# Optimization experiments

Measured on AMD Instinct MI355X. Metric: run time of the kernel, lower is better.

Reference implementation:

```python
import jax, jax.numpy as jnp
import numpy as np

B, T, SD, NE = 4, 2048, 64, 4096   # batch, block_size, sqrt_d, n_embd (= SD*SD)
H, HS = 8, 8                        # n_head, head_size (H*HS == SD)
FH = 4 * SD                         # FFN hidden
EPS = 1e-5


def setup_inputs() -> dict:
    key = jax.random.key(0)
    ks = jax.random.split(key, 17)
    s = 0.05  # linear-layer init scale
    return {
        "x": jax.random.normal(ks[0], (B, T, NE), jnp.float32),
        # Feebler / Booster weights: torch.randn in original
        "feebler_w": jax.random.normal(ks[1], (SD, SD, T), jnp.float32),
        "booster_w": jax.random.normal(ks[2], (SD, SD, T), jnp.float32),
        # per-head q/k/v projections (no bias): applied as y @ W -> (B,T,HS)
        "wq": jax.random.normal(ks[3], (H, SD, HS), jnp.float32) * s,
        "wk": jax.random.normal(ks[4], (H, SD, HS), jnp.float32) * s,
        "wv": jax.random.normal(ks[5], (H, SD, HS), jnp.float32) * s,
        "proj_w": jax.random.normal(ks[6], (SD, SD), jnp.float32) * s,
        "proj_b": jnp.zeros((SD,), jnp.float32),
        "ln1_g": jnp.ones((SD,), jnp.float32),
        "ln1_b": jnp.zeros((SD,), jnp.float32),
        "ln2_g": jnp.ones((SD,), jnp.float32),
        "ln2_b": jnp.zeros((SD,), jnp.float32),
        "w1": jax.random.normal(ks[7], (SD, FH), jnp.float32) * s,
        "b1": jnp.zeros((FH,), jnp.float32),
        "w2": jax.random.normal(ks[8], (FH, SD), jnp.float32) * s,
        "b2": jnp.zeros((SD,), jnp.float32),
    }


def _layer_norm(x, g, b):
    m = jnp.mean(x, axis=-1, keepdims=True)
    v = jnp.mean((x - m) ** 2, axis=-1, keepdims=True)
    return (x - m) * jax.lax.rsqrt(v + EPS) * g + b


def reference(x, feebler_w, booster_w, wq, wk, wv, proj_w, proj_b,
              ln1_g, ln1_b, ln2_g, ln2_b, w1, b1, w2, b2):
    # ---- Feebler: (B,T,NE) flat-reshaped to (B,SD,SD,T), mul weights, sum dim 2
    xr = x.reshape(B, SD, SD, T)                     # flat reinterpretation (torch .view)
    h = jnp.einsum('bijt,ijt->bit', xr, feebler_w)   # (B, SD, T)
    h = h.reshape(B, T, SD)                          # flat reinterpretation, NOT transpose

    # ---- QuickHead multi-head 'attention' (sum-pooled elementwise)
    y = _layer_norm(h, ln1_g, ln1_b)                 # (B, T, SD)
    q = jnp.einsum('bts,hsd->bhtd', y, wq)           # (B, H, T, HS)
    k = jnp.einsum('bts,hsd->bhtd', y, wk)
    v = jnp.einsum('bts,hsd->bhtd', y, wv)
    ck = jnp.sum(k, axis=2, keepdims=True)           # (B, H, 1, HS)
    cv = jnp.sum(v, axis=2, keepdims=True)
    aw = jax.nn.softmax(q * ck, axis=2)              # softmax over T
    sa = cv * aw                                     # (B, H, T, HS)
    sa = jnp.transpose(sa, (0, 2, 1, 3)).reshape(B, T, SD)  # concat heads
    sa = sa @ proj_w + proj_b                        # proj (dropout = identity, eval)
    h = h + sa

    # ---- FeedForward
    y2 = _layer_norm(h, ln2_g, ln2_b)
    f = jax.nn.relu(y2 @ w1 + b1) @ w2 + b2
    h = h + f

    # ---- Booster: broadcast-multiply against (SD,SD,T) weights
    hr = h.reshape(B, SD, T)                         # flat reinterpretation
    rev = booster_w[None, :, :, :] * hr[:, None, :, :]  # (B, SD, SD, T)
    return rev.reshape(B, T, NE)                     # flat reinterpretation
```

## Files before the change

kernel.cpp:

```cpp
#include <hip/hip_runtime.h>
#include <hip/hip_bf16.h>


#define EPSF 1e-5f
#define OFFS 40.0f

__global__ void K1(const float* __restrict__ x, const float* __restrict__ fw,
                   const float* __restrict__ g, const float* __restrict__ bia,
                   float* __restrict__ h, float* __restrict__ y,
                   float* __restrict__ part) {
    int bid = blockIdx.x;
    int xcd = bid & 7, slot = bid >> 3;
    int b = slot & 3;
    int panel = (slot >> 2) * 8 + xcd;
    int i = panel & 63, chunk = panel >> 6;
    int t4 = chunk * 256 + threadIdx.x;
    const float4* x4 = (const float4*)x + (size_t)b * 2097152 + (size_t)i * 32768 + t4;
    const float4* f4 = (const float4*)fw + (size_t)i * 32768 + t4;
    float4 acc = make_float4(0.f, 0.f, 0.f, 0.f);
    #pragma unroll 8
    for (int j = 0; j < 64; ++j) {
        float4 xv = x4[(size_t)j * 512];
        float4 fv = f4[(size_t)j * 512];
        acc.x += xv.x * fv.x; acc.y += xv.y * fv.y;
        acc.z += xv.z * fv.z; acc.w += xv.w * fv.w;
    }
    float s1 = acc.x + acc.y + acc.z + acc.w;
    float s2 = acc.x * acc.x + acc.y * acc.y + acc.z * acc.z + acc.w * acc.w;
    for (int off = 8; off; off >>= 1) {
        s1 += __shfl_xor(s1, off);
        s2 += __shfl_xor(s2, off);
    }
    float m = s1 * (1.f / 64.f);
    float var = s2 * (1.f / 64.f) - m * m;
    float rs = rsqrtf(var + EPSF);
    float4 gv = ((const float4*)g)[t4 & 15];
    float4 bv = ((const float4*)bia)[t4 & 15];
    float4 yv;
    yv.x = (acc.x - m) * rs * gv.x + bv.x;
    yv.y = (acc.y - m) * rs * gv.y + bv.y;
    yv.z = (acc.z - m) * rs * gv.z + bv.z;
    yv.w = (acc.w - m) * rs * gv.w + bv.w;
    size_t oidx = (size_t)b * 32768 + (size_t)i * 512 + t4;
    ((float4*)h)[oidx] = acc;
    ((float4*)y)[oidx] = yv;
    __shared__ float ysL[64];
    if (threadIdx.x < 64) ysL[threadIdx.x] = 0.f;
    __syncthreads();
    int c0 = (t4 & 15) * 4;
    atomicAdd(&ysL[c0 + 0], yv.x);
    atomicAdd(&ysL[c0 + 1], yv.y);
    atomicAdd(&ysL[c0 + 2], yv.z);
    atomicAdd(&ysL[c0 + 3], yv.w);
    __syncthreads();
    if (threadIdx.x < 64)
        part[(panel * 4 + b) * 64 + threadIdx.x] = ysL[threadIdx.x];
}

__global__ void K2(const float* __restrict__ y, const float* __restrict__ wq,
                   const float* __restrict__ wk, const float* __restrict__ part,
                   float* __restrict__ e, float* __restrict__ esum) {
    __shared__ float yT[64][20];
    __shared__ float wqL[64][64];
    __shared__ float psum[4][64];
    __shared__ float psA[4][64];
    __shared__ float ysL[64];
    int b = blockIdx.x, tile = blockIdx.y, t0 = tile * 16;
    int tid = threadIdx.x;
    int c = tid & 63, grp = tid >> 6;
    float sA = 0.f;
    for (int pp = 0; pp < 32; ++pp)
        sA += part[((grp * 32 + pp) * 4 + b) * 64 + c];
    psA[grp][c] = sA;
    for (int k = 0; k < 4; ++k) {
        int idx = k * 256 + tid;
        int r = idx >> 6, s = idx & 63;
        yT[s][r] = y[(size_t)b * 131072 + (size_t)(t0 + r) * 64 + s];
    }
    for (int k = 0; k < 16; ++k) {
        int idx = k * 256 + tid;
        int r = idx >> 6, cc = idx & 63;
        wqL[r][cc] = wq[(cc >> 3) * 512 + r * 8 + (cc & 7)];
    }
    __syncthreads();
    if (tid < 64)
        ysL[tid] = psA[0][tid] + psA[1][tid] + psA[2][tid] + psA[3][tid];
    __syncthreads();
    float ckc = 0.f;
    for (int s = 0; s < 64; ++s)
        ckc += ysL[s] * wk[(c >> 3) * 512 + s * 8 + (c & 7)];
    float acc[4] = {0.f, 0.f, 0.f, 0.f};
    for (int s = 0; s < 64; ++s) {
        float w = wqL[s][c];
        float4 a0 = *(const float4*)&yT[s][grp * 4];
        acc[0] += a0.x * w; acc[1] += a0.y * w;
        acc[2] += a0.z * w; acc[3] += a0.w * w;
    }
    float ls = 0.f;
    #pragma unroll
    for (int k = 0; k < 4; ++k) {
        float v = __expf(acc[k] * ckc - OFFS);
        e[(size_t)b * 131072 + (size_t)(t0 + grp * 4 + k) * 64 + c] = v;
        ls += v;
    }
    psum[grp][c] = ls;
    __syncthreads();
    if (tid < 64)
        esum[(b * 128 + tile) * 64 + tid] =
            psum[0][tid] + psum[1][tid] + psum[2][tid] + psum[3][tid];
}

__global__ void __launch_bounds__(256, 3)
K3m(const float* __restrict__ h, const float* __restrict__ e,
    const float* __restrict__ part, const float* __restrict__ esum,
    const float* __restrict__ wv, const float* __restrict__ projw,
    const float* __restrict__ projb, const float* __restrict__ g2,
    const float* __restrict__ b2l, const float* __restrict__ w1,
    const float* __restrict__ b1, const float* __restrict__ w2,
    const float* __restrict__ fb2, float* __restrict__ hf) {
    __shared__ float bufA[4096];
    __shared__ float bufB[4096];
    __shared__ float4 pT[4][64];
    __shared__ float4 y2T[4][64];
    __shared__ float4 hidT[4][64];
    __shared__ float psA[4][64], psE[4][64];
    __shared__ float ysL[64], denL[64];
    int b = blockIdx.x, chunk = blockIdx.y;
    int tid = threadIdx.x, l = tid & 63, w = tid >> 6;

    float4* bufA4 = (float4*)bufA;
    const float4* pw4 = (const float4*)projw;
    #pragma unroll
    for (int k = 0; k < 4; ++k) bufA4[k * 256 + tid] = pw4[k * 256 + tid];
    float sA = 0.f, sE = 0.f;
    for (int pp = 0; pp < 32; ++pp) {
        sA += part[((w * 32 + pp) * 4 + b) * 64 + l];
        sE += esum[(b * 128 + w * 32 + pp) * 64 + l];
    }
    psA[w][l] = sA;
    psE[w][l] = sE;
    __syncthreads();
    if (tid < 64) {
        ysL[tid] = psA[0][tid] + psA[1][tid] + psA[2][tid] + psA[3][tid];
        denL[tid] = psE[0][tid] + psE[1][tid] + psE[2][tid] + psE[3][tid];
    }
    __syncthreads();
    float cvv = 0.f;
    for (int s = 0; s < 64; ++s)
        cvv += ysL[s] * wv[(l >> 3) * 512 + s * 8 + (l & 7)];
    float sc = cvv / denL[l];

    size_t base = (size_t)b * 131072 + (size_t)(chunk * 16 + w * 4) * 64 + l;
    float4 p;
    p.x = e[base] * sc;
    p.y = e[base + 64] * sc;
    p.z = e[base + 128] * sc;
    p.w = e[base + 192] * sc;
    pT[w][l] = p;
    float h0 = h[base], h1r = h[base + 64], h2r = h[base + 128], h3r = h[base + 192];
    __syncthreads();

    float a[4] = {0.f, 0.f, 0.f, 0.f};
    for (int c = 0; c < 64; ++c) {
        float4 pv = pT[w][c];
        float pw = bufA[c * 64 + l];
        a[0] += pv.x * pw; a[1] += pv.y * pw;
        a[2] += pv.z * pw; a[3] += pv.w * pw;
    }
    float pb = projb[l], g2v = g2[l], b2v = b2l[l];
    float hmid[4] = {h0 + a[0] + pb, h1r + a[1] + pb, h2r + a[2] + pb, h3r + a[3] + pb};
    float y2[4];
    #pragma unroll
    for (int rr = 0; rr < 4; ++rr) {
        float v = hmid[rr];
        float s1 = v, s2 = v * v;
        for (int off = 32; off; off >>= 1) {
            s1 += __shfl_xor(s1, off);
            s2 += __shfl_xor(s2, off);
        }
        float mm = s1 * (1.f / 64.f);
        float var = s2 * (1.f / 64.f) - mm * mm;
        float rs = rsqrtf(var + EPSF);
        y2[rr] = (v - mm) * rs * g2v + b2v;
    }
    y2T[w][l] = make_float4(y2[0], y2[1], y2[2], y2[3]);
    __syncthreads();

    float4* bufB4 = (float4*)bufB;
    const float4* w14 = (const float4*)w1;
    const float4* w24 = (const float4*)w2;
    float a2[4] = {0.f, 0.f, 0.f, 0.f};
    for (int c4 = 0; c4 < 4; ++c4) {
        #pragma unroll
        for (int k = 0; k < 4; ++k) {
            int f = k * 256 + tid;
            int r = f >> 4, q = f & 15;
            bufA4[r * 16 + q] = w14[r * 64 + c4 * 16 + q];
            bufB4[r * 16 + q] = w24[(size_t)(c4 * 64 + r) * 16 + q];
        }
        __syncthreads();
        float bb = b1[c4 * 64 + l];
        float hc[4] = {bb, bb, bb, bb};
        for (int s = 0; s < 64; ++s) {
            float4 yv = y2T[w][s];
            float w1v = bufA[s * 64 + l];
            hc[0] += yv.x * w1v; hc[1] += yv.y * w1v;
            hc[2] += yv.z * w1v; hc[3] += yv.w * w1v;
        }
        hidT[w][l] = make_float4(fmaxf(hc[0], 0.f), fmaxf(hc[1], 0.f),
                                 fmaxf(hc[2], 0.f), fmaxf(hc[3], 0.f));
        for (int j = 0; j < 64; ++j) {
            float4 hv = hidT[w][j];
            float w2v = bufB[j * 64 + l];
            a2[0] += hv.x * w2v; a2[1] += hv.y * w2v;
            a2[2] += hv.z * w2v; a2[3] += hv.w * w2v;
        }
        __syncthreads();
    }
    float fb = fb2[l];
    hf[base]       = hmid[0] + a2[0] + fb;
    hf[base + 64]  = hmid[1] + a2[1] + fb;
    hf[base + 128] = hmid[2] + a2[2] + fb;
    hf[base + 192] = hmid[3] + a2[3] + fb;
}

__global__ void K5(const float* __restrict__ hf, const float* __restrict__ bw,
                   float* __restrict__ out) {
    int wi = blockIdx.x * 256 + threadIdx.x;
    int i = wi >> 15;
    int jt = wi & 32767;
    const float4* bw4 = (const float4*)bw;
    const float4* hf4 = (const float4*)hf;
    float4* o4 = (float4*)out;
    float4 wv = bw4[wi];
    size_t obase = (size_t)i * 32768 + jt;
    #pragma unroll
    for (int b = 0; b < 4; ++b) {
        float4 hv = hf4[b * 32768 + jt];
        float4 ov;
        ov.x = wv.x * hv.x; ov.y = wv.y * hv.y;
        ov.z = wv.z * hv.z; ov.w = wv.w * hv.w;
        o4[(size_t)b * 2097152 + obase] = ov;
    }
}

extern "C" void kernel_launch(void* const* d_in, const int* in_sizes, int n_in,
                              void* d_out, int out_size, void* d_ws, size_t ws_size,
                              hipStream_t stream) {
    const float* x     = (const float*)d_in[0];
    const float* fw    = (const float*)d_in[1];
    const float* bw    = (const float*)d_in[2];
    const float* wq    = (const float*)d_in[3];
    const float* wk    = (const float*)d_in[4];
    const float* wv    = (const float*)d_in[5];
    const float* projw = (const float*)d_in[6];
    const float* projb = (const float*)d_in[7];
    const float* g1    = (const float*)d_in[8];
    const float* b1l   = (const float*)d_in[9];
    const float* g2    = (const float*)d_in[10];
    const float* b2l   = (const float*)d_in[11];
    const float* w1    = (const float*)d_in[12];
    const float* b1    = (const float*)d_in[13];
    const float* w2    = (const float*)d_in[14];
    const float* b2    = (const float*)d_in[15];
    float* out = (float*)d_out;

    float* wsf = (float*)d_ws;
    float* h    = wsf;
    float* y    = wsf + 524288;
    float* hf   = wsf + 524288;
    float* e    = wsf + 1048576;
    float* part = wsf + 1572864;
    float* esum = wsf + 1605632;

    K1 <<<512, 256, 0, stream>>>(x, fw, g1, b1l, h, y, part);
    K2 <<<dim3(4, 128), 256, 0, stream>>>(y, wq, wk, part, e, esum);
    K3m<<<dim3(4, 128), 256, 0, stream>>>(h, e, part, esum, wv, projw, projb,
                                          g2, b2l, w1, b1, w2, b2, hf);
    K5 <<<8192, 256, 0, stream>>>(hf, bw, out);
}
```

Before: 140.3 us.

## Replace partial-sum buffers with global atomics and widen K3 blocks

K1 and K2 now add their per-block column sums straight into small global accumulators with atomics, where before they wrote partial arrays that K2 and K3 each re-reduced over 128 entries. A memset is added to clear these accumulators. K3 goes from 256 to 512 threads per block, each block handling 32 rows instead of 16, so half as many blocks reload the proj/w1/w2 weights into shared memory. The cost is float atomic contention and a non-deterministic summation order.

```diff
diff --git a/kernel.cpp b/kernel.cpp
--- a/kernel.cpp
+++ b/kernel.cpp
@@ -8,7 +8,7 @@
 __global__ void K1(const float* __restrict__ x, const float* __restrict__ fw,
                    const float* __restrict__ g, const float* __restrict__ bia,
                    float* __restrict__ h, float* __restrict__ y,
-                   float* __restrict__ part) {
+                   float* __restrict__ ysumG) {
     int bid = blockIdx.x;
     int xcd = bid & 7, slot = bid >> 3;
     int b = slot & 3;
@@ -54,24 +54,20 @@
     atomicAdd(&ysL[c0 + 3], yv.w);
     __syncthreads();
     if (threadIdx.x < 64)
-        part[(panel * 4 + b) * 64 + threadIdx.x] = ysL[threadIdx.x];
+        atomicAdd(&ysumG[b * 64 + threadIdx.x], ysL[threadIdx.x]);
 }
 
 __global__ void K2(const float* __restrict__ y, const float* __restrict__ wq,
-                   const float* __restrict__ wk, const float* __restrict__ part,
-                   float* __restrict__ e, float* __restrict__ esum) {
+                   const float* __restrict__ wk, const float* __restrict__ ysumG,
+                   float* __restrict__ e, float* __restrict__ denG) {
     __shared__ float yT[64][20];
     __shared__ float wqL[64][64];
     __shared__ float psum[4][64];
-    __shared__ float psA[4][64];
-    __shared__ float ysL[64];
+    __shared__ float ysS[64];
     int b = blockIdx.x, tile = blockIdx.y, t0 = tile * 16;
     int tid = threadIdx.x;
     int c = tid & 63, grp = tid >> 6;
-    float sA = 0.f;
-    for (int pp = 0; pp < 32; ++pp)
-        sA += part[((grp * 32 + pp) * 4 + b) * 64 + c];
-    psA[grp][c] = sA;
+    if (tid < 64) ysS[tid] = ysumG[b * 64 + tid];
     for (int k = 0; k < 4; ++k) {
         int idx = k * 256 + tid;
         int r = idx >> 6, s = idx & 63;
@@ -83,12 +79,9 @@
         wqL[r][cc] = wq[(cc >> 3) * 512 + r * 8 + (cc & 7)];
     }
     __syncthreads();
-    if (tid < 64)
-        ysL[tid] = psA[0][tid] + psA[1][tid] + psA[2][tid] + psA[3][tid];
-    __syncthreads();
     float ckc = 0.f;
     for (int s = 0; s < 64; ++s)
-        ckc += ysL[s] * wk[(c >> 3) * 512 + s * 8 + (c & 7)];
+        ckc += ysS[s] * wk[(c >> 3) * 512 + s * 8 + (c & 7)];
     float acc[4] = {0.f, 0.f, 0.f, 0.f};
     for (int s = 0; s < 64; ++s) {
         float w = wqL[s][c];
@@ -106,58 +99,45 @@
     psum[grp][c] = ls;
     __syncthreads();
     if (tid < 64)
-        esum[(b * 128 + tile) * 64 + tid] =
-            psum[0][tid] + psum[1][tid] + psum[2][tid] + psum[3][tid];
-}
-
-__global__ void __launch_bounds__(256, 3)
-K3m(const float* __restrict__ h, const float* __restrict__ e,
-    const float* __restrict__ part, const float* __restrict__ esum,
-    const float* __restrict__ wv, const float* __restrict__ projw,
-    const float* __restrict__ projb, const float* __restrict__ g2,
-    const float* __restrict__ b2l, const float* __restrict__ w1,
-    const float* __restrict__ b1, const float* __restrict__ w2,
-    const float* __restrict__ fb2, float* __restrict__ hf) {
+        atomicAdd(&denG[b * 64 + tid],
+                  psum[0][tid] + psum[1][tid] + psum[2][tid] + psum[3][tid]);
+}
+
+__global__ void __launch_bounds__(512, 4)
+K3(const float* __restrict__ h, const float* __restrict__ e,
+   const float* __restrict__ ysumG, const float* __restrict__ denG,
+   const float* __restrict__ wv, const float* __restrict__ projw,
+   const float* __restrict__ projb, const float* __restrict__ g2,
+   const float* __restrict__ b2l, const float* __restrict__ w1,
+   const float* __restrict__ b1, const float* __restrict__ w2,
+   const float* __restrict__ fb2, float* __restrict__ hf) {
     __shared__ float bufA[4096];
     __shared__ float bufB[4096];
-    __shared__ float4 pT[4][64];
-    __shared__ float4 y2T[4][64];
-    __shared__ float4 hidT[4][64];
-    __shared__ float psA[4][64], psE[4][64];
-    __shared__ float ysL[64], denL[64];
+    __shared__ float4 pT[8][64];
+    __shared__ float4 y2T[8][64];
+    __shared__ float4 hidT[8][64];
+    __shared__ float ysS[64], sclS[64];
     int b = blockIdx.x, chunk = blockIdx.y;
     int tid = threadIdx.x, l = tid & 63, w = tid >> 6;
 
     float4* bufA4 = (float4*)bufA;
     const float4* pw4 = (const float4*)projw;
-    #pragma unroll
-    for (int k = 0; k < 4; ++k) bufA4[k * 256 + tid] = pw4[k * 256 + tid];
-    float sA = 0.f, sE = 0.f;
-    for (int pp = 0; pp < 32; ++pp) {
-        sA += part[((w * 32 + pp) * 4 + b) * 64 + l];
-        sE += esum[(b * 128 + w * 32 + pp) * 64 + l];
-    }
-    psA[w][l] = sA;
-    psE[w][l] = sE;
+    bufA4[tid] = pw4[tid];
+    bufA4[512 + tid] = pw4[512 + tid];
+    if (tid < 64) ysS[tid] = ysumG[b * 64 + tid];
+    size_t base = (size_t)b * 131072 + (size_t)(chunk * 32 + w * 4) * 64 + l;
+    float e0 = e[base], e1 = e[base + 64], e2 = e[base + 128], e3 = e[base + 192];
+    float h0 = h[base], h1r = h[base + 64], h2r = h[base + 128], h3r = h[base + 192];
     __syncthreads();
     if (tid < 64) {
-        ysL[tid] = psA[0][tid] + psA[1][tid] + psA[2][tid] + psA[3][tid];
-        denL[tid] = psE[0][tid] + psE[1][tid] + psE[2][tid] + psE[3][tid];
-    }
-    __syncthreads();
-    float cvv = 0.f;
-    for (int s = 0; s < 64; ++s)
-        cvv += ysL[s] * wv[(l >> 3) * 512 + s * 8 + (l & 7)];
-    float sc = cvv / denL[l];
-
-    size_t base = (size_t)b * 131072 + (size_t)(chunk * 16 + w * 4) * 64 + l;
-    float4 p;
-    p.x = e[base] * sc;
-    p.y = e[base + 64] * sc;
-    p.z = e[base + 128] * sc;
-    p.w = e[base + 192] * sc;
-    pT[w][l] = p;
-    float h0 = h[base], h1r = h[base + 64], h2r = h[base + 128], h3r = h[base + 192];
+        float cvv = 0.f;
+        for (int s = 0; s < 64; ++s)
+            cvv += ysS[s] * wv[(tid >> 3) * 512 + s * 8 + (tid & 7)];
+        sclS[tid] = cvv / denG[b * 64 + tid];
+    }
+    __syncthreads();
+    float sc = sclS[l];
+    pT[w][l] = make_float4(e0 * sc, e1 * sc, e2 * sc, e3 * sc);
     __syncthreads();
 
     float a[4] = {0.f, 0.f, 0.f, 0.f};
@@ -192,8 +172,8 @@
     float a2[4] = {0.f, 0.f, 0.f, 0.f};
     for (int c4 = 0; c4 < 4; ++c4) {
         #pragma unroll
-        for (int k = 0; k < 4; ++k) {
-            int f = k * 256 + tid;
+        for (int k = 0; k < 2; ++k) {
+            int f = k * 512 + tid;
             int r = f >> 4, q = f & 15;
             bufA4[r * 16 + q] = w14[r * 64 + c4 * 16 + q];
             bufB4[r * 16 + q] = w24[(size_t)(c4 * 64 + r) * 16 + q];
@@ -266,16 +246,18 @@
     float* out = (float*)d_out;
 
     float* wsf = (float*)d_ws;
-    float* h    = wsf;
-    float* y    = wsf + 524288;
-    float* hf   = wsf + 524288;
-    float* e    = wsf + 1048576;
-    float* part = wsf + 1572864;
-    float* esum = wsf + 1605632;
-
-    K1 <<<512, 256, 0, stream>>>(x, fw, g1, b1l, h, y, part);
-    K2 <<<dim3(4, 128), 256, 0, stream>>>(y, wq, wk, part, e, esum);
-    K3m<<<dim3(4, 128), 256, 0, stream>>>(h, e, part, esum, wv, projw, projb,
-                                          g2, b2l, w1, b1, w2, b2, hf);
-    K5 <<<8192, 256, 0, stream>>>(hf, bw, out);
-}
+    float* h     = wsf;
+    float* y     = wsf + 524288;
+    float* hf    = wsf + 524288;
+    float* e     = wsf + 1048576;
+    float* ysumG = wsf + 1572864;
+    float* denG  = wsf + 1573120;
+
+    hipMemsetAsync(ysumG, 0, 512 * sizeof(float), stream);
+
+    K1<<<512, 256, 0, stream>>>(x, fw, g1, b1l, h, y, ysumG);
+    K2<<<dim3(4, 128), 256, 0, stream>>>(y, wq, wk, ysumG, e, denG);
+    K3<<<dim3(4, 64), 512, 0, stream>>>(h, e, ysumG, denG, wv, projw, projb,
+                                        g2, b2l, w1, b1, w2, b2, hf);
+    K5<<<8192, 256, 0, stream>>>(hf, bw, out);
+}
```

After: 143.5 us. +2.3%, slower.
